# Optimization experiments

Measured on AMD Instinct MI355X. Metric: run time of the kernel, lower is better.

Reference implementation:

```python
import jax, jax.numpy as jnp
import numpy as np

B_, L, D_MODEL = 8, 2048, 512
EXPAND, D_STATE, HEADDIM, NGROUPS, D_CONV = 2, 16, 64, 1, 4
D_INNER = EXPAND * D_MODEL            # 1024
NHEADS = D_INNER // HEADDIM           # 16
CONV_DIM = D_INNER + 2 * NGROUPS * D_STATE   # 1056
D_IN_PROJ = 2 * D_INNER + 2 * NGROUPS * D_STATE + NHEADS  # 2096
EPS = 1e-5


def _mamba_params(key):
    ks = jax.random.split(key, 5)
    in_proj_w = jax.random.normal(ks[0], (D_IN_PROJ, D_MODEL), jnp.float32) * (D_MODEL ** -0.5)
    conv_w = jax.random.normal(ks[1], (CONV_DIM, 1, D_CONV), jnp.float32) * (D_CONV ** -0.5)
    conv_b = jnp.zeros((CONV_DIM,), jnp.float32)
    # inverse-softplus of dt ~ U[1e-3, 0.1] (mamba-ssm style init)
    dt_bias = jnp.log(jnp.expm1(jax.random.uniform(ks[2], (NHEADS,), jnp.float32, 1e-3, 0.1)))
    A_log = jnp.log(jax.random.uniform(ks[3], (NHEADS,), jnp.float32, 1.0, 16.0))
    Dp = jnp.ones((NHEADS,), jnp.float32)
    norm_w = jnp.ones((D_INNER,), jnp.float32)
    out_proj_w = jax.random.normal(ks[4], (D_MODEL, D_INNER), jnp.float32) * (D_INNER ** -0.5)
    return [in_proj_w, conv_w, conv_b, dt_bias, A_log, Dp, norm_w, out_proj_w]


def setup_inputs() -> dict:
    key = jax.random.key(0)
    k0, k1, k2 = jax.random.split(key, 3)
    d = {"x": jax.random.normal(k0, (B_, L, D_MODEL), jnp.float32)}
    names = ["in_proj_w", "conv_w", "conv_b", "dt_bias", "A_log", "Dp", "norm_w", "out_proj_w"]
    for pre, k in (("fwd_", k1), ("bwd_", k2)):
        for n, p in zip(names, _mamba_params(k)):
            d[pre + n] = p
    return d


def _silu(v):
    return v * jax.nn.sigmoid(v)


def _mamba2(u, in_proj_w, conv_w, conv_b, dt_bias, A_log, Dp, norm_w, out_proj_w):
    b, l, _ = u.shape
    zxbcdt = u @ in_proj_w.T                                # (b,l,D_IN_PROJ)
    z, xBC, dt = jnp.split(zxbcdt, [D_INNER, D_INNER + CONV_DIM], axis=-1)
    # causal depthwise conv1d + silu
    xc = jnp.transpose(xBC, (0, 2, 1))                      # (b,C,l)
    xc = jax.lax.conv_general_dilated(xc, conv_w, (1,), [(D_CONV - 1, 0)],
                                      feature_group_count=CONV_DIM)
    xBC = _silu(jnp.transpose(xc, (0, 2, 1)) + conv_b)      # (b,l,C)
    xs, Bm, Cm = jnp.split(xBC, [D_INNER, D_INNER + NGROUPS * D_STATE], axis=-1)
    xs = xs.reshape(b, l, NHEADS, HEADDIM)
    Bm = Bm.reshape(b, l, NGROUPS, D_STATE)[:, :, 0]        # ngroups=1 -> (b,l,N)
    Cm = Cm.reshape(b, l, NGROUPS, D_STATE)[:, :, 0]
    dt = jax.nn.softplus(dt + dt_bias)                      # (b,l,H)
    A = -jnp.exp(A_log)                                     # (H,)
    dA = jnp.exp(dt * A)                                    # (b,l,H), in (0,1)

    def step(h, inp):
        dA_t, dt_t, x_t, B_t, C_t = inp
        h = h * dA_t[:, :, None, None] + jnp.einsum('bh,bhp,bn->bhpn', dt_t, x_t, B_t)
        y = jnp.einsum('bhpn,bn->bhp', h, C_t)
        return h, y

    h0 = jnp.zeros((b, NHEADS, HEADDIM, D_STATE), u.dtype)
    seq = (jnp.moveaxis(dA, 1, 0), jnp.moveaxis(dt, 1, 0), jnp.moveaxis(xs, 1, 0),
           jnp.moveaxis(Bm, 1, 0), jnp.moveaxis(Cm, 1, 0))
    _, ys = jax.lax.scan(step, h0, seq)
    y = jnp.moveaxis(ys, 0, 1) + xs * Dp[None, None, :, None]   # (b,l,H,P)
    y = y.reshape(b, l, D_INNER)
    # RMSNormGated (norm_before_gate=False): rmsnorm(y * silu(z)) * w
    y = y * _silu(z)
    y = y * jax.lax.rsqrt(jnp.mean(y * y, axis=-1, keepdims=True) + EPS) * norm_w
    return y @ out_proj_w.T


def reference(x,
              fwd_in_proj_w, fwd_conv_w, fwd_conv_b, fwd_dt_bias, fwd_A_log, fwd_Dp, fwd_norm_w, fwd_out_proj_w,
              bwd_in_proj_w, bwd_conv_w, bwd_conv_b, bwd_dt_bias, bwd_A_log, bwd_Dp, bwd_norm_w, bwd_out_proj_w):
    fwd = _mamba2(x, fwd_in_proj_w, fwd_conv_w, fwd_conv_b, fwd_dt_bias, fwd_A_log, fwd_Dp, fwd_norm_w, fwd_out_proj_w)
    bwd = _mamba2(x[:, ::-1], bwd_in_proj_w, bwd_conv_w, bwd_conv_b, bwd_dt_bias, bwd_A_log, bwd_Dp, bwd_norm_w, bwd_out_proj_w)
    return fwd + bwd[:, ::-1]
```

## Files before the change

### kernel.cpp

```cpp
#include <hip/hip_runtime.h>
#include <stdint.h>

#define L_SEQ   2048
#define BATCH   8
#define DMODEL  512
#define DINNER  1024
#define NHEADS  16
#define HEADDIM 64
#define DSTATE  16
#define CONVDIM 1056
#define DINPROJ 2096
#define NPROJ   4192
#define NPROJ_P 4224
#define NROWS   (BATCH*L_SEQ)
#define NCH     16
#define CHLEN   128
#define XBCW    1072

typedef __attribute__((ext_vector_type(8))) short short8;
typedef __attribute__((ext_vector_type(4))) float f32x4;

static __device__ __forceinline__ unsigned short f2bf(float f) {
    unsigned int u = __float_as_uint(f);
    u += 0x7FFF + ((u >> 16) & 1);
    return (unsigned short)(u >> 16);
}
static __device__ __forceinline__ float bf2f(unsigned short u) {
    return __uint_as_float((unsigned int)u << 16);
}
static __device__ __forceinline__ float silu(float v) {
    return v / (1.f + __expf(-v));
}
static __device__ __forceinline__ void glds16(const unsigned short* g, unsigned short* l) {
    __builtin_amdgcn_global_load_lds(
        (const __attribute__((address_space(1))) unsigned int*)g,
        (__attribute__((address_space(3))) unsigned int*)l, 16, 0, 0);
}

#define PREP_N1 (NROWS*DMODEL)
#define PREP_N2 (NPROJ_P*DMODEL)
#define PREP_N3 (512*2048)
__global__ void k_prep(const float* __restrict__ x,
                       const float* __restrict__ fwi, const float* __restrict__ bwi,
                       const float* __restrict__ fow, const float* __restrict__ bow,
                       unsigned short* __restrict__ XB, unsigned short* __restrict__ W1,
                       unsigned short* __restrict__ W2) {
    int i = blockIdx.x * 256 + threadIdx.x;
    if (i < PREP_N1) {
        XB[i] = f2bf(x[i]);
    } else if (i < PREP_N1 + PREP_N2) {
        int j = i - PREP_N1;
        const int FS = DINPROJ * DMODEL;
        W1[j] = (j < 2 * FS) ? f2bf(j < FS ? fwi[j] : bwi[j - FS]) : 0;
    } else if (i < PREP_N1 + PREP_N2 + PREP_N3) {
        int j = i - PREP_N1 - PREP_N2;
        int n = j >> 11, k = j & 2047;
        float v = (k < DINNER) ? fow[n * DINNER + k] : bow[n * DINNER + k - DINNER];
        W2[j] = f2bf(v);
    }
}

#define BM 128
#define BN 128
#define BK 32

#define GEMM_BODY(NROUNDS, EPILOGUE)                                                        \
    __shared__ __align__(16) unsigned short as[2][BM][BK];                                  \
    __shared__ __align__(16) unsigned short bs[2][BN][BK];                                  \
    const int tid = threadIdx.x;                                                            \
    const int lane = tid & 63;                                                              \
    const int wave = tid >> 6;                                                              \
    const int wm = (wave & 1) * 64;                                                         \
    const int wn = (wave >> 1) * 64;                                                        \
    const int l16 = lane & 15;                                                              \
    const int q = lane >> 4;                                                                \
    const int sr = wave * 32;                                                               \
    const int lr = lane >> 2;                                                               \
    const int lc = (lane & 3) * 8;                                                          \
    f32x4 acc[4][4];                                                                        \
    for (int i = 0; i < 4; i++)                                                             \
        for (int j = 0; j < 4; j++) acc[i][j] = (f32x4){0.f, 0.f, 0.f, 0.f};                \
    const unsigned short* Ab = A + (size_t)(bm + sr + lr) * K + koff + lc;                  \
    const unsigned short* Bb = Bw + (size_t)(bn + sr + lr) * K + koff + lc;                 \
    glds16(Ab, &as[0][sr][0]);                                                              \
    glds16(Ab + (size_t)16 * K, &as[0][sr + 16][0]);                                        \
    glds16(Bb, &bs[0][sr][0]);                                                              \
    glds16(Bb + (size_t)16 * K, &bs[0][sr + 16][0]);                                        \
    __syncthreads();                                                                        \
    for (int r = 0; r < NROUNDS; r++) {                                                     \
        const int pb = r & 1;                                                               \
        if (r + 1 < NROUNDS) {               \
            const int kb = (r + 1) * BK;                                                    \
            glds16(Ab + kb, &as[pb ^ 1][sr][0]);                                            \
            glds16(Ab + (size_t)16 * K + kb, &as[pb ^ 1][sr + 16][0]);                      \
            glds16(Bb + kb, &bs[pb ^ 1][sr][0]);                                            \
            glds16(Bb + (size_t)16 * K + kb, &bs[pb ^ 1][sr + 16][0]);                      \
        }                                                                                   \
        short8 af[4], bfr[4];                                                               \
        for (int i = 0; i < 4; i++) af[i] = *(const short8*)&as[pb][wm + i * 16 + l16][q * 8]; \
        for (int j = 0; j < 4; j++) bfr[j] = *(const short8*)&bs[pb][wn + j * 16 + l16][q * 8]; \
        for (int i = 0; i < 4; i++)                                                         \
            for (int j = 0; j < 4; j++)                                                     \
                acc[i][j] = __builtin_amdgcn_mfma_f32_16x16x32_bf16(af[i], bfr[j], acc[i][j], 0, 0, 0); \
        __syncthreads();             \
    }                                                                                       \
    EPILOGUE

__global__ __launch_bounds__(256) void k_gemm_proj(const unsigned short* __restrict__ A,
                                                   const unsigned short* __restrict__ Bw,
                                                   unsigned short* __restrict__ ZG,
                                                   unsigned short* __restrict__ XBCDT) {
    const int K = DMODEL;
    const int N = NPROJ;
    const int lin = blockIdx.x;
    const int xcd = lin & 7;
    const int idx = lin >> 3;
    const int mloc = idx & 15;
    const int n_tile = idx >> 4;
    const int bm = (mloc * 8 + xcd) * BM;
    const int bn = n_tile * BN;
    const int koff = 0;
    GEMM_BODY(16, {
        for (int i = 0; i < 4; i++) {
            int row0 = bm + wm + i * 16 + q * 4;
            for (int j = 0; j < 4; j++) {
                int col = bn + wn + j * 16 + l16;
                if (col < N) {
                    int dir = col >= DINPROJ;
                    int cc = col - dir * DINPROJ;
                    for (int r = 0; r < 4; r++) {
                        unsigned short v = f2bf(acc[i][j][r]);
                        size_t rowo = (size_t)(dir * NROWS + row0 + r);
                        if (cc < DINNER)
                            ZG[rowo * DINNER + cc] = v;
                        else
                            XBCDT[rowo * XBCW + (cc - DINNER)] = v;
                    }
                }
            }
        }
    })
}

__global__ __launch_bounds__(256) void k_gemm_out(const unsigned short* __restrict__ A,
                                                  const unsigned short* __restrict__ Bw,
                                                  float* __restrict__ C0,
                                                  float* __restrict__ C1) {
    const int K = 2048;
    const int N = 512;
    const int lin = blockIdx.x;
    const int xcd = lin & 7;
    const int idx = lin >> 3;
    const int ksplit = idx >> 6;
    const int rem = idx & 63;
    const int g = rem >> 4;
    const int r2 = rem & 15;
    const int n_tile = r2 >> 2;
    const int mloc = (g << 2) | (r2 & 3);
    const int bm = (mloc * 8 + xcd) * BM;
    const int bn = n_tile * BN;
    const int koff = ksplit * 1024;
    float* __restrict__ C = ksplit ? C1 : C0;
    GEMM_BODY(32, {
        for (int i = 0; i < 4; i++) {
            int row0 = bm + wm + i * 16 + q * 4;
            for (int j = 0; j < 4; j++) {
                int col = bn + wn + j * 16 + l16;
                for (int r = 0; r < 4; r++)
                    C[(size_t)(row0 + r) * N + col] = acc[i][j][r];
            }
        }
    })
}

__global__ void k_addout(float* __restrict__ C0, const float* __restrict__ C1) {
    int i = blockIdx.x * 256 + threadIdx.x;
    if (i < NROWS * 512 / 4) {
        f32x4 a = *(const f32x4*)&C0[i * 4];
        f32x4 b = *(const f32x4*)&C1[i * 4];
        a += b;
        *(f32x4*)&C0[i * 4] = a;
    }
}

__global__ __launch_bounds__(256) void k_conv2(const unsigned short* __restrict__ XBCDT,
                                               const float* __restrict__ fw_w, const float* __restrict__ fw_b,
                                               const float* __restrict__ bw_w, const float* __restrict__ bw_b,
                                               unsigned short* __restrict__ XS, float* __restrict__ BCb) {
    __shared__ unsigned short sm[70][256];
    int t = threadIdx.x;
    int bidx = blockIdx.x;
    int lcn = bidx & 31;
    int b   = (bidx >> 5) & 7;
    int dir = (bidx >> 8) & 1;
    int ct  = bidx >> 9;
    int c0 = ct * 256;
    int l0 = lcn * 64;
    int c = c0 + t;
    const unsigned short* src = XBCDT + (size_t)dir * NROWS * XBCW;
    bool cok = (c < CONVDIM);
#pragma unroll 2
    for (int r = 0; r < 70; r++) {
        int li = l0 - 3 + r;
        unsigned short v = 0;
        if (li >= 0 && li < L_SEQ && cok)
            v = src[(size_t)((b << 11) + li) * XBCW + c];
        sm[r][t] = v;
    }
    __syncthreads();
    if (!cok) return;
    const float* w = (dir ? bw_w : fw_w) + c * 4;
    float bias = (dir ? bw_b : fw_b)[c];
    float wr[4];
    if (dir) { wr[0] = w[3]; wr[1] = w[2]; wr[2] = w[1]; wr[3] = w[0]; }
    else     { wr[0] = w[0]; wr[1] = w[1]; wr[2] = w[2]; wr[3] = w[3]; }
    int o = dir ? 3 : 0;
    float w0 = bf2f(sm[o][t]), w1 = bf2f(sm[o + 1][t]), w2 = bf2f(sm[o + 2][t]);
    unsigned short* xso = XS + (size_t)dir * NROWS * DINNER;
    float* bco = BCb + (size_t)dir * NROWS * 32;
    int rowbase = (b << 11) + l0;
#pragma unroll 4
    for (int l = 0; l < 64; l++) {
        float w3 = bf2f(sm[l + o + 3][t]);
        float acc = ((wr[0] * w0 + wr[1] * w1) + (wr[2] * w2 + wr[3] * w3)) + bias;
        float v = silu(acc);
        int row = rowbase + l;
        if (c < DINNER)
            xso[(size_t)row * DINNER + c] = f2bf(v);
        else
            bco[(size_t)row * 32 + (c - DINNER)] = v;
        w0 = w1; w1 = w2; w2 = w3;
    }
}

__global__ void k_dt(const unsigned short* __restrict__ XBCDT,
                     const float* __restrict__ fdtb, const float* __restrict__ fAl,
                     const float* __restrict__ bdtb, const float* __restrict__ bAl,
                     float* __restrict__ DT, float* __restrict__ DA) {
    int gid = blockIdx.x * 256 + threadIdx.x;
    if (gid >= 2 * NROWS * NHEADS) return;
    int h = gid & 15;
    int row = (gid >> 4) & (NROWS - 1);
    int dir = gid >> 18;
    float dtb = (dir ? bdtb : fdtb)[h];
    float Al = (dir ? bAl : fAl)[h];
    float x = bf2f(XBCDT[(size_t)(dir * NROWS + row) * XBCW + CONVDIM + h]) + dtb;
    float dt = (x > 15.f) ? x : log1pf(__expf(x));
    float dA = __expf(-__expf(Al) * dt);
    DT[gid] = dt;
    DA[gid] = dA;
}

__global__ __launch_bounds__(64) void k_scan_state(const unsigned short* __restrict__ XS,
                                                   const float* __restrict__ BCb,
                                                   const float* __restrict__ DT,
                                                   const float* __restrict__ DA,
                                                   float* __restrict__ S, float* __restrict__ P) {
    int idx = blockIdx.x;
    int c = idx & 15, h = (idx >> 4) & 15, b = (idx >> 8) & 7, dir = idx >> 11;
    int p = threadIdx.x;
    const unsigned short* xs = XS + (size_t)dir * NROWS * DINNER;
    const float* bc = BCb + (size_t)dir * NROWS * 32;
    const float* dtp = DT + (size_t)dir * NROWS * NHEADS;
    const float* dap = DA + (size_t)dir * NROWS * NHEADS;
    float hreg[16];
#pragma unroll
    for (int n = 0; n < 16; n++) hreg[n] = 0.f;
    float Pp = 1.f;
#pragma unroll 4
    for (int tl = 0; tl < CHLEN; ++tl) {
        int t = c * CHLEN + tl;
        int l = dir ? (L_SEQ - 1 - t) : t;
        int row = (b << 11) + l;
        float xv = bf2f(xs[(size_t)row * DINNER + h * HEADDIM + p]);
        float dt = dtp[row * 16 + h];
        float dA = dap[row * 16 + h];
        f32x4 Bv[4];
#pragma unroll
        for (int qq = 0; qq < 4; qq++) Bv[qq] = *(const f32x4*)&bc[(size_t)row * 32 + qq * 4];
        float kk = dt * xv;
#pragma unroll
        for (int n = 0; n < 16; n++) hreg[n] = fmaf(hreg[n], dA, kk * Bv[n >> 2][n & 3]);
        Pp *= dA;
    }
#pragma unroll
    for (int qq = 0; qq < 4; qq++) {
        f32x4 v = {hreg[qq * 4], hreg[qq * 4 + 1], hreg[qq * 4 + 2], hreg[qq * 4 + 3]};
        *(f32x4*)&S[(size_t)idx * 1024 + p * 16 + qq * 4] = v;
    }
    if (p == 0) P[idx] = Pp;
}

__global__ void k_combine(float* __restrict__ S, const float* __restrict__ P) {
    int gid = blockIdx.x * 256 + threadIdx.x;
    if (gid >= 2 * 8 * 16 * 1024) return;
    int pn = gid & 1023;
    int base = gid >> 10;
    float H = 0.f;
#pragma unroll 4
    for (int c = 0; c < NCH; c++) {
        size_t o = ((size_t)base * NCH + c) * 1024 + pn;
        float s = S[o];
        S[o] = H;
        H = H * P[base * NCH + c] + s;
    }
}

__global__ __launch_bounds__(64) void k_scan_out(const unsigned short* __restrict__ XS,
                                                 const float* __restrict__ BCb,
                                                 const float* __restrict__ DT,
                                                 const float* __restrict__ DA,
                                                 const float* __restrict__ Hinit,
                                                 const float* __restrict__ fDp,
                                                 const float* __restrict__ bDp,
                                                 unsigned short* __restrict__ Y) {
    int idx = blockIdx.x;
    int c = idx & 15, h = (idx >> 4) & 15, b = (idx >> 8) & 7, dir = idx >> 11;
    int p = threadIdx.x;
    const unsigned short* xs = XS + (size_t)dir * NROWS * DINNER;
    const float* bc = BCb + (size_t)dir * NROWS * 32;
    const float* dtp = DT + (size_t)dir * NROWS * NHEADS;
    const float* dap = DA + (size_t)dir * NROWS * NHEADS;
    unsigned short* yo = Y + (size_t)dir * NROWS * DINNER;
    float Dpv = (dir ? bDp : fDp)[h];
    float hreg[16];
#pragma unroll
    for (int qq = 0; qq < 4; qq++) {
        f32x4 v = *(const f32x4*)&Hinit[(size_t)idx * 1024 + p * 16 + qq * 4];
#pragma unroll
        for (int e = 0; e < 4; e++) hreg[qq * 4 + e] = v[e];
    }
#pragma unroll 4
    for (int tl = 0; tl < CHLEN; ++tl) {
        int t = c * CHLEN + tl;
        int l = dir ? (L_SEQ - 1 - t) : t;
        int row = (b << 11) + l;
        float xv = bf2f(xs[(size_t)row * DINNER + h * HEADDIM + p]);
        float dt = dtp[row * 16 + h];
        float dA = dap[row * 16 + h];
        f32x4 Bv[4], Cv[4];
#pragma unroll
        for (int qq = 0; qq < 4; qq++) Bv[qq] = *(const f32x4*)&bc[(size_t)row * 32 + qq * 4];
#pragma unroll
        for (int qq = 0; qq < 4; qq++) Cv[qq] = *(const f32x4*)&bc[(size_t)row * 32 + 16 + qq * 4];
        float kk = dt * xv;
        float y = 0.f;
#pragma unroll
        for (int n = 0; n < 16; n++) {
            hreg[n] = fmaf(hreg[n], dA, kk * Bv[n >> 2][n & 3]);
            y = fmaf(hreg[n], Cv[n >> 2][n & 3], y);
        }
        yo[(size_t)row * DINNER + h * HEADDIM + p] = f2bf(y + xv * Dpv);
    }
}

__global__ __launch_bounds__(256) void k_gatenorm(const unsigned short* __restrict__ Y,
                                                  const unsigned short* __restrict__ ZG,
                                                  const float* __restrict__ fnw,
                                                  const float* __restrict__ bnw,
                                                  unsigned short* __restrict__ NRM) {
    int bid = blockIdx.x;
    int dir = bid >> 14;
    int row = bid & (NROWS - 1);
    int tid = threadIdx.x;
    int c = tid * 4;
    ushort4 yu = *(const ushort4*)&Y[(size_t)(dir * NROWS + row) * DINNER + c];
    ushort4 zu = *(const ushort4*)&ZG[(size_t)(dir * NROWS + row) * DINNER + c];
    float v0 = bf2f(yu.x) * silu(bf2f(zu.x));
    float v1 = bf2f(yu.y) * silu(bf2f(zu.y));
    float v2 = bf2f(yu.z) * silu(bf2f(zu.z));
    float v3 = bf2f(yu.w) * silu(bf2f(zu.w));
    float ss = v0 * v0 + v1 * v1 + v2 * v2 + v3 * v3;
#pragma unroll
    for (int off = 32; off > 0; off >>= 1) ss += __shfl_down(ss, off);
    __shared__ float red[4];
    if ((tid & 63) == 0) red[tid >> 6] = ss;
    __syncthreads();
    float tot = red[0] + red[1] + red[2] + red[3];
    float scale = rsqrtf(tot * (1.f / 1024.f) + 1e-5f);
    const float* nw = dir ? bnw : fnw;
    ushort4 o;
    o.x = f2bf(v0 * scale * nw[c]);
    o.y = f2bf(v1 * scale * nw[c + 1]);
    o.z = f2bf(v2 * scale * nw[c + 2]);
    o.w = f2bf(v3 * scale * nw[c + 3]);
    *(ushort4*)&NRM[(size_t)row * 2048 + dir * DINNER + c] = o;
}

extern "C" void kernel_launch(void* const* d_in, const int* in_sizes, int n_in,
                              void* d_out, int out_size, void* d_ws, size_t ws_size,
                              hipStream_t stream) {
    const float* x     = (const float*)d_in[0];
    const float* f_inw = (const float*)d_in[1];
    const float* f_cw  = (const float*)d_in[2];
    const float* f_cb  = (const float*)d_in[3];
    const float* f_dtb = (const float*)d_in[4];
    const float* f_Al  = (const float*)d_in[5];
    const float* f_Dp  = (const float*)d_in[6];
    const float* f_nw  = (const float*)d_in[7];
    const float* f_ow  = (const float*)d_in[8];
    const float* b_inw = (const float*)d_in[9];
    const float* b_cw  = (const float*)d_in[10];
    const float* b_cb  = (const float*)d_in[11];
    const float* b_dtb = (const float*)d_in[12];
    const float* b_Al  = (const float*)d_in[13];
    const float* b_Dp  = (const float*)d_in[14];
    const float* b_nw  = (const float*)d_in[15];
    const float* b_ow  = (const float*)d_in[16];

    char* ws = (char*)d_ws;
    size_t off = 0;
    auto alloc = [&](size_t bytes) {
        void* p = ws + off;
        off += (bytes + 255) & ~(size_t)255;
        return p;
    };
    unsigned short* XBCDT = (unsigned short*)alloc((size_t)2 * NROWS * XBCW * 2);
    unsigned short* NRM   = XBCDT;
    unsigned short* XS    = (unsigned short*)alloc((size_t)2 * NROWS * DINNER * 2);
    unsigned short* Yb    = XS;
    unsigned short* ZG    = (unsigned short*)alloc((size_t)2 * NROWS * DINNER * 2);
    float* PBUF = (float*)ZG;
    unsigned short* W2    = (unsigned short*)alloc((size_t)512 * 2048 * 2);
    float* BCb  = (float*)alloc((size_t)2 * NROWS * 32 * 4);
    float* DT   = (float*)alloc((size_t)2 * NROWS * NHEADS * 4);
    float* DA   = (float*)alloc((size_t)2 * NROWS * NHEADS * 4);
    char* unionBase = (char*)alloc((size_t)16777216 + (size_t)NPROJ_P * DMODEL * 2);
    unsigned short* XB = (unsigned short*)unionBase;
    unsigned short* W1 = (unsigned short*)(unionBase + 16777216);
    float* S = (float*)unionBase;
    float* P = (float*)(unionBase + 16777216);

    if (ws_size < off) return;

    {
        int n = PREP_N1 + PREP_N2 + PREP_N3;
        k_prep<<<(n + 255) / 256, 256, 0, stream>>>(x, f_inw, b_inw, f_ow, b_ow, XB, W1, W2);
    }
    k_gemm_proj<<<8 * 16 * 33, 256, 0, stream>>>(XB, W1, ZG, XBCDT);
    k_conv2<<<5 * 2 * 8 * 32, 256, 0, stream>>>(XBCDT, f_cw, f_cb, b_cw, b_cb, XS, BCb);
    {
        int n = 2 * NROWS * NHEADS;
        k_dt<<<(n + 255) / 256, 256, 0, stream>>>(XBCDT, f_dtb, f_Al, b_dtb, b_Al, DT, DA);
    }
    k_scan_state<<<2 * 8 * 16 * NCH, 64, 0, stream>>>(XS, BCb, DT, DA, S, P);
    {
        int n = 2 * 8 * 16 * 1024;
        k_combine<<<(n + 255) / 256, 256, 0, stream>>>(S, P);
    }
    k_scan_out<<<2 * 8 * 16 * NCH, 64, 0, stream>>>(XS, BCb, DT, DA, S, f_Dp, b_Dp, Yb);
    k_gatenorm<<<2 * NROWS, 256, 0, stream>>>(Yb, ZG, f_nw, b_nw, NRM);
    k_gemm_out<<<8 * 128, 256, 0, stream>>>(NRM, W2, (float*)d_out, PBUF);
    {
        int n = NROWS * 512 / 4;
        k_addout<<<(n + 255) / 256, 256, 0, stream>>>((float*)d_out, PBUF);
    }
}
```

Measured before the change: 556.7 us.

## Halve GEMM M-tile, drop split-K out-proj, vectorize gate-norm two rows per block

Shrinks the shared GEMM tile from 128x128 to 64x128, doubling the block count for both projections. The output projection no longer uses split-K with a partial buffer and a separate add kernel; it does the full K=2048 loop per block and writes directly. The gate-norm kernel now handles two rows per 256-thread block with 8-element vector loads and stores. The aim is to remove the add pass and its extra traffic and to improve load balance, at the cost of less operand reuse per tile.

```diff
diff --git a/kernel.cpp b/kernel.cpp
--- a/kernel.cpp
+++ b/kernel.cpp
@@ -60,7 +60,7 @@
     }
 }
 
-#define BM 128
+#define BM 64
 #define BN 128
 #define BK 32
 
@@ -70,39 +70,38 @@
     const int tid = threadIdx.x;                                                            \
     const int lane = tid & 63;                                                              \
     const int wave = tid >> 6;                                                              \
-    const int wm = (wave & 1) * 64;                                                         \
+    const int wm = (wave & 1) * 32;                                                         \
     const int wn = (wave >> 1) * 64;                                                        \
     const int l16 = lane & 15;                                                              \
     const int q = lane >> 4;                                                                \
-    const int sr = wave * 32;                                                               \
+    const int sra = wave * 16;                                                              \
+    const int srb = wave * 32;                                                              \
     const int lr = lane >> 2;                                                               \
     const int lc = (lane & 3) * 8;                                                          \
-    f32x4 acc[4][4];                                                                        \
-    for (int i = 0; i < 4; i++)                                                             \
+    f32x4 acc[2][4];                                                                        \
+    for (int i = 0; i < 2; i++)                                                             \
         for (int j = 0; j < 4; j++) acc[i][j] = (f32x4){0.f, 0.f, 0.f, 0.f};                \
-    const unsigned short* Ab = A + (size_t)(bm + sr + lr) * K + koff + lc;                  \
-    const unsigned short* Bb = Bw + (size_t)(bn + sr + lr) * K + koff + lc;                 \
-    glds16(Ab, &as[0][sr][0]);                                                              \
-    glds16(Ab + (size_t)16 * K, &as[0][sr + 16][0]);                                        \
-    glds16(Bb, &bs[0][sr][0]);                                                              \
-    glds16(Bb + (size_t)16 * K, &bs[0][sr + 16][0]);                                        \
+    const unsigned short* Ab = A + (size_t)(bm + sra + lr) * K + koff + lc;                 \
+    const unsigned short* Bb = Bw + (size_t)(bn + srb + lr) * K + koff + lc;                \
+    glds16(Ab, &as[0][sra][0]);                                                             \
+    glds16(Bb, &bs[0][srb][0]);                                                             \
+    glds16(Bb + (size_t)16 * K, &bs[0][srb + 16][0]);                                       \
     __syncthreads();                                                                        \
     for (int r = 0; r < NROUNDS; r++) {                                                     \
         const int pb = r & 1;                                                               \
         if (r + 1 < NROUNDS) {               \
             const int kb = (r + 1) * BK;                                                    \
-            glds16(Ab + kb, &as[pb ^ 1][sr][0]);                                            \
-            glds16(Ab + (size_t)16 * K + kb, &as[pb ^ 1][sr + 16][0]);                      \
-            glds16(Bb + kb, &bs[pb ^ 1][sr][0]);                                            \
-            glds16(Bb + (size_t)16 * K + kb, &bs[pb ^ 1][sr + 16][0]);                      \
+            glds16(Ab + kb, &as[pb ^ 1][sra][0]);                                           \
+            glds16(Bb + kb, &bs[pb ^ 1][srb][0]);                                           \
+            glds16(Bb + (size_t)16 * K + kb, &bs[pb ^ 1][srb + 16][0]);                     \
         }                                                                                   \
-        short8 af[4], bfr[4];                                                               \
-        for (int i = 0; i < 4; i++) af[i] = *(const short8*)&as[pb][wm + i * 16 + l16][q * 8]; \
+        short8 af[2], bfr[4];                                                               \
+        for (int i = 0; i < 2; i++) af[i] = *(const short8*)&as[pb][wm + i * 16 + l16][q * 8]; \
         for (int j = 0; j < 4; j++) bfr[j] = *(const short8*)&bs[pb][wn + j * 16 + l16][q * 8]; \
-        for (int i = 0; i < 4; i++)                                                         \
+        for (int i = 0; i < 2; i++)                                                         \
             for (int j = 0; j < 4; j++)                                                     \
                 acc[i][j] = __builtin_amdgcn_mfma_f32_16x16x32_bf16(af[i], bfr[j], acc[i][j], 0, 0, 0); \
-        __syncthreads();             \
+        __syncthreads();            \
     }                                                                                       \
     EPILOGUE
 
@@ -115,13 +114,13 @@
     const int lin = blockIdx.x;
     const int xcd = lin & 7;
     const int idx = lin >> 3;
-    const int mloc = idx & 15;
-    const int n_tile = idx >> 4;
+    const int mloc = idx & 31;
+    const int n_tile = idx >> 5;
     const int bm = (mloc * 8 + xcd) * BM;
     const int bn = n_tile * BN;
     const int koff = 0;
     GEMM_BODY(16, {
-        for (int i = 0; i < 4; i++) {
+        for (int i = 0; i < 2; i++) {
             int row0 = bm + wm + i * 16 + q * 4;
             for (int j = 0; j < 4; j++) {
                 int col = bn + wn + j * 16 + l16;
@@ -144,43 +143,26 @@
 
 __global__ __launch_bounds__(256) void k_gemm_out(const unsigned short* __restrict__ A,
                                                   const unsigned short* __restrict__ Bw,
-                                                  float* __restrict__ C0,
-                                                  float* __restrict__ C1) {
+                                                  float* __restrict__ C) {
     const int K = 2048;
-    const int N = 512;
     const int lin = blockIdx.x;
     const int xcd = lin & 7;
     const int idx = lin >> 3;
-    const int ksplit = idx >> 6;
-    const int rem = idx & 63;
-    const int g = rem >> 4;
-    const int r2 = rem & 15;
-    const int n_tile = r2 >> 2;
-    const int mloc = (g << 2) | (r2 & 3);
+    const int mloc = idx & 31;
+    const int n_tile = idx >> 5;
     const int bm = (mloc * 8 + xcd) * BM;
     const int bn = n_tile * BN;
-    const int koff = ksplit * 1024;
-    float* __restrict__ C = ksplit ? C1 : C0;
-    GEMM_BODY(32, {
-        for (int i = 0; i < 4; i++) {
+    const int koff = 0;
+    GEMM_BODY(64, {
+        for (int i = 0; i < 2; i++) {
             int row0 = bm + wm + i * 16 + q * 4;
             for (int j = 0; j < 4; j++) {
                 int col = bn + wn + j * 16 + l16;
                 for (int r = 0; r < 4; r++)
-                    C[(size_t)(row0 + r) * N + col] = acc[i][j][r];
+                    C[(size_t)(row0 + r) * 512 + col] = acc[i][j][r];
             }
         }
     })
-}
-
-__global__ void k_addout(float* __restrict__ C0, const float* __restrict__ C1) {
-    int i = blockIdx.x * 256 + threadIdx.x;
-    if (i < NROWS * 512 / 4) {
-        f32x4 a = *(const f32x4*)&C0[i * 4];
-        f32x4 b = *(const f32x4*)&C1[i * 4];
-        a += b;
-        *(f32x4*)&C0[i * 4] = a;
-    }
 }
 
 __global__ __launch_bounds__(256) void k_conv2(const unsigned short* __restrict__ XBCDT,
@@ -360,31 +342,48 @@
                                                   const float* __restrict__ bnw,
                                                   unsigned short* __restrict__ NRM) {
     int bid = blockIdx.x;
-    int dir = bid >> 14;
-    int row = bid & (NROWS - 1);
-    int tid = threadIdx.x;
-    int c = tid * 4;
-    ushort4 yu = *(const ushort4*)&Y[(size_t)(dir * NROWS + row) * DINNER + c];
-    ushort4 zu = *(const ushort4*)&ZG[(size_t)(dir * NROWS + row) * DINNER + c];
-    float v0 = bf2f(yu.x) * silu(bf2f(zu.x));
-    float v1 = bf2f(yu.y) * silu(bf2f(zu.y));
-    float v2 = bf2f(yu.z) * silu(bf2f(zu.z));
-    float v3 = bf2f(yu.w) * silu(bf2f(zu.w));
-    float ss = v0 * v0 + v1 * v1 + v2 * v2 + v3 * v3;
+    int t = threadIdx.x;
+    int sub = t >> 7;
+    int tt = t & 127;
+    int rid = bid * 2 + sub;
+    int dir = rid >> 14;
+    int row = rid & (NROWS - 1);
+    int c = tt * 8;
+    const size_t base = (size_t)(dir * NROWS + row) * DINNER + c;
+    uint4 yu = *(const uint4*)&Y[base];
+    uint4 zu = *(const uint4*)&ZG[base];
+    float v[8];
+    {
+        const unsigned int yw[4] = {yu.x, yu.y, yu.z, yu.w};
+        const unsigned int zw[4] = {zu.x, zu.y, zu.z, zu.w};
+#pragma unroll
+        for (int e = 0; e < 4; e++) {
+            v[e * 2]     = bf2f((unsigned short)(yw[e] & 0xffff)) * silu(bf2f((unsigned short)(zw[e] & 0xffff)));
+            v[e * 2 + 1] = bf2f((unsigned short)(yw[e] >> 16))    * silu(bf2f((unsigned short)(zw[e] >> 16)));
+        }
+    }
+    float ss = 0.f;
+#pragma unroll
+    for (int e = 0; e < 8; e++) ss += v[e] * v[e];
 #pragma unroll
     for (int off = 32; off > 0; off >>= 1) ss += __shfl_down(ss, off);
     __shared__ float red[4];
-    if ((tid & 63) == 0) red[tid >> 6] = ss;
+    if ((t & 63) == 0) red[t >> 6] = ss;
     __syncthreads();
-    float tot = red[0] + red[1] + red[2] + red[3];
+    float tot = red[sub * 2] + red[sub * 2 + 1];
     float scale = rsqrtf(tot * (1.f / 1024.f) + 1e-5f);
-    const float* nw = dir ? bnw : fnw;
-    ushort4 o;
-    o.x = f2bf(v0 * scale * nw[c]);
-    o.y = f2bf(v1 * scale * nw[c + 1]);
-    o.z = f2bf(v2 * scale * nw[c + 2]);
-    o.w = f2bf(v3 * scale * nw[c + 3]);
-    *(ushort4*)&NRM[(size_t)row * 2048 + dir * DINNER + c] = o;
+    const float* nw = (dir ? bnw : fnw) + c;
+    f32x4 nw0 = *(const f32x4*)&nw[0];
+    f32x4 nw1 = *(const f32x4*)&nw[4];
+    unsigned int ow[4];
+#pragma unroll
+    for (int e = 0; e < 4; e++) {
+        float a = v[e * 2]     * scale * (e < 2 ? nw0[e * 2]     : nw1[(e - 2) * 2]);
+        float b = v[e * 2 + 1] * scale * (e < 2 ? nw0[e * 2 + 1] : nw1[(e - 2) * 2 + 1]);
+        ow[e] = (unsigned int)f2bf(a) | ((unsigned int)f2bf(b) << 16);
+    }
+    uint4 o = {ow[0], ow[1], ow[2], ow[3]};
+    *(uint4*)&NRM[(size_t)row * 2048 + dir * DINNER + c] = o;
 }
 
 extern "C" void kernel_launch(void* const* d_in, const int* in_sizes, int n_in,
@@ -420,7 +419,6 @@
     unsigned short* XS    = (unsigned short*)alloc((size_t)2 * NROWS * DINNER * 2);
     unsigned short* Yb    = XS;
     unsigned short* ZG    = (unsigned short*)alloc((size_t)2 * NROWS * DINNER * 2);
-    float* PBUF = (float*)ZG;
     unsigned short* W2    = (unsigned short*)alloc((size_t)512 * 2048 * 2);
     float* BCb  = (float*)alloc((size_t)2 * NROWS * 32 * 4);
     float* DT   = (float*)alloc((size_t)2 * NROWS * NHEADS * 4);
@@ -437,7 +435,7 @@
         int n = PREP_N1 + PREP_N2 + PREP_N3;
         k_prep<<<(n + 255) / 256, 256, 0, stream>>>(x, f_inw, b_inw, f_ow, b_ow, XB, W1, W2);
     }
-    k_gemm_proj<<<8 * 16 * 33, 256, 0, stream>>>(XB, W1, ZG, XBCDT);
+    k_gemm_proj<<<8 * 32 * 33, 256, 0, stream>>>(XB, W1, ZG, XBCDT);
     k_conv2<<<5 * 2 * 8 * 32, 256, 0, stream>>>(XBCDT, f_cw, f_cb, b_cw, b_cb, XS, BCb);
     {
         int n = 2 * NROWS * NHEADS;
@@ -449,10 +447,6 @@
         k_combine<<<(n + 255) / 256, 256, 0, stream>>>(S, P);
     }
     k_scan_out<<<2 * 8 * 16 * NCH, 64, 0, stream>>>(XS, BCb, DT, DA, S, f_Dp, b_Dp, Yb);
-    k_gatenorm<<<2 * NROWS, 256, 0, stream>>>(Yb, ZG, f_nw, b_nw, NRM);
-    k_gemm_out<<<8 * 128, 256, 0, stream>>>(NRM, W2, (float*)d_out, PBUF);
-    {
-        int n = NROWS * 512 / 4;
-        k_addout<<<(n + 255) / 256, 256, 0, stream>>>((float*)d_out, PBUF);
-    }
-}
+    k_gatenorm<<<NROWS, 256, 0, stream>>>(Yb, ZG, f_nw, b_nw, NRM);
+    k_gemm_out<<<8 * 32 * 4, 256, 0, stream>>>(NRM, W2, (float*)d_out);
+}
```

New measurement: 551.1 us. Within noise of the previous version (-1.0%).
